# Performance work log

Measured on AMD Instinct MI355X. Metric: run time of the kernel, lower is better.

Reference implementation:

```python
import jax, jax.numpy as jnp
import numpy as np

N = 8192          # nodes
E = 262144        # edges (avg degree 32)
IN = 32           # output_seq_len * in_channels
HID = 16          # hidden_channels
HEADS = 8
OUT = 32          # output_seq_len * out_channels
SLOPE = 0.2       # GATv2 leaky_relu negative_slope
EPS = 1e-12       # F.normalize eps


def setup_inputs() -> dict:
    key = jax.random.key(0)
    ks = jax.random.split(key, 12)
    g = lambda k, shape, fan: (jax.random.normal(k, shape, jnp.float32) / np.float32(np.sqrt(fan)))
    x = jax.random.normal(ks[0], (N, IN), jnp.float32)
    edge_index = jax.random.randint(ks[1], (2, E), 0, N, dtype=jnp.int64)
    # conv1: in=IN -> HEADS x HID, concat
    W1l = g(ks[2], (IN, HEADS * HID), IN)
    b1l = jnp.zeros((HEADS * HID,), jnp.float32)
    W1r = g(ks[3], (IN, HEADS * HID), IN)
    b1r = jnp.zeros((HEADS * HID,), jnp.float32)
    att1 = g(ks[4], (HEADS, HID), HID)
    bias1 = jnp.zeros((HEADS * HID,), jnp.float32)
    W2l = g(ks[5], (HEADS * HID, OUT), HEADS * HID)
    b2l = jnp.zeros((OUT,), jnp.float32)
    W2r = g(ks[6], (HEADS * HID, OUT), HEADS * HID)
    b2r = jnp.zeros((OUT,), jnp.float32)
    att2 = g(ks[7], (1, OUT), OUT)
    bias2 = jnp.zeros((OUT,), jnp.float32)
    return {"x": x, "edge_index": edge_index,
            "W1l": W1l, "b1l": b1l, "W1r": W1r, "b1r": b1r, "att1": att1, "bias1": bias1,
            "W2l": W2l, "b2l": b2l, "W2r": W2r, "b2r": b2r, "att2": att2, "bias2": bias2}


def gatv2_conv(x, src, dst, Wl, bl, Wr, br, att, bias, heads, C, concat):
    """GATv2Conv (eval mode, self-loops already in src/dst). x: [N, F]."""
    n = x.shape[0]
    xl = (x @ Wl + bl).reshape(n, heads, C)  # source transform
    xr = (x @ Wr + br).reshape(n, heads, C)  # target transform
    h = jax.nn.leaky_relu(xl[src] + xr[dst], SLOPE)        # [Etot, H, C]
    e = jnp.einsum('ehc,hc->eh', h, att)                    # [Etot, H]
    m = jax.ops.segment_max(e, dst, num_segments=n)         # stable softmax per target
    p = jnp.exp(e - m[dst])
    s = jax.ops.segment_sum(p, dst, num_segments=n)
    alpha = p / (s[dst] + 1e-16)                            # [Etot, H]
    out = jax.ops.segment_sum(alpha[:, :, None] * xl[src], dst, num_segments=n)  # [n, H, C]
    out = out.reshape(n, heads * C) if concat else out.mean(axis=1)
    return out + bias


def reference(x, edge_index, W1l, b1l, W1r, b1r, att1, bias1, W2l, b2l, W2r, b2r, att2, bias2):
    n = x.shape[0]
    loops = jnp.arange(n, dtype=edge_index.dtype)
    src = jnp.concatenate([edge_index[0], loops])
    dst = jnp.concatenate([edge_index[1], loops])
    h1 = gatv2_conv(x, src, dst, W1l, b1l, W1r, b1r, att1, bias1, HEADS, HID, True)
    h2 = gatv2_conv(h1, src, dst, W2l, b2l, W2r, b2r, att2, bias2, 1, OUT, False)
    norm = jnp.sqrt(jnp.sum(h2 * h2, axis=1, keepdims=True))
    z = h2 / jnp.maximum(norm, EPS)                         # F.normalize(p=2, dim=1)
    A_pred = jax.nn.sigmoid(z @ z.T)                        # [N, N]
    return (A_pred, z)
```

## Files before the change

### kernel.cpp

```cpp
#include <hip/hip_runtime.h>
#include <hip/hip_bf16.h>
#include <cstdint>
#include <cstddef>

typedef float f32x4 __attribute__((ext_vector_type(4)));
typedef short short8 __attribute__((ext_vector_type(8)));

#define SLOT_SHIFT 7

__device__ __forceinline__ float bf2f(ushort u){ return __uint_as_float(((unsigned)u) << 16); }
__device__ __forceinline__ float lrelu(float v){ return fmaxf(v, 0.2f*v); }

__global__ __launch_bounds__(128) void k_linear1(const float* __restrict__ x,
                          const float* __restrict__ W1l, const float* __restrict__ b1l,
                          const float* __restrict__ W1r, const float* __restrict__ b1r,
                          __hip_bfloat16* __restrict__ xl1b, float* __restrict__ xr1,
                          int* __restrict__ cur, int N){
  __shared__ float xs[16][32];
  int t = threadIdx.x;
  int gid = blockIdx.x*128 + t;
  if (gid < N) cur[gid] = gid << SLOT_SHIFT;
  int r0 = blockIdx.x * 16;
  float wl[32], wr[32];
  #pragma unroll
  for (int k = 0; k < 32; k++){ wl[k] = W1l[k*128 + t]; wr[k] = W1r[k*128 + t]; }
  float bl = b1l[t], br = b1r[t];
  #pragma unroll
  for (int i = 0; i < 4; i++){
    int idx = t + i*128;
    xs[idx >> 5][idx & 31] = x[r0*32 + idx];
  }
  __syncthreads();
  #pragma unroll 4
  for (int r = 0; r < 16; r++){
    float al = bl, ar = br;
    const float4* xv4 = (const float4*)xs[r];
    #pragma unroll
    for (int q = 0; q < 8; q++){
      float4 xv = xv4[q];
      al += xv.x*wl[q*4+0] + xv.y*wl[q*4+1] + xv.z*wl[q*4+2] + xv.w*wl[q*4+3];
      ar += xv.x*wr[q*4+0] + xv.y*wr[q*4+1] + xv.z*wr[q*4+2] + xv.w*wr[q*4+3];
    }
    xl1b[(size_t)(r0+r)*128 + t] = __float2bfloat16(al);
    xr1[(size_t)(r0+r)*128 + t] = ar;
  }
}

__global__ void k_scatter(const int* __restrict__ ei, int E, int N,
                          int* __restrict__ cur, int* __restrict__ ssrc){
  int i = blockIdx.x*blockDim.x + threadIdx.x;
  int tot = E + N;
  if (i >= tot) return;
  int s = (i < E) ? ei[i]     : (i - E);
  int d = (i < E) ? ei[E + i] : (i - E);
  int pos = atomicAdd(&cur[d], 1);
  ssrc[pos] = s;
}

__global__ __launch_bounds__(256) void k_conv1l2(const int* __restrict__ cur,
                       const int* __restrict__ ssrc,
                       const __hip_bfloat16* __restrict__ xl1b, const float* __restrict__ xr1,
                       const float* __restrict__ att1, const float* __restrict__ bias1,
                       const float* __restrict__ W2l, const float* __restrict__ b2l,
                       const float* __restrict__ W2r, const float* __restrict__ b2r,
                       __hip_bfloat16* __restrict__ xl2b, float* __restrict__ xr2){
  __shared__ float p_s[2][128][8];
  __shared__ float h1s[8][128];
  int t = threadIdx.x;
  int sub = t >> 7, f = t & 127;
  int hp = f & 7;
  const ushort* xb = (const ushort*)xl1b;
  float4 attr0 = *(const float4*)(att1 + hp*16);
  float4 attr1 = *(const float4*)(att1 + hp*16 + 4);
  float4 attr2 = *(const float4*)(att1 + hp*16 + 8);
  float4 attr3 = *(const float4*)(att1 + hp*16 + 12);
  float b1f = bias1[f];
  int d0 = blockIdx.x*8;
  #pragma unroll
  for (int it = 0; it < 4; it++){
    int d = d0 + it*2 + sub;
    int j0 = d << SLOT_SHIFT;
    int deg = cur[d] - j0;
    float4 xr0 = *(const float4*)(xr1 + (size_t)d*128 + hp*16);
    float4 xr1v = *(const float4*)(xr1 + (size_t)d*128 + hp*16 + 4);
    float4 xr2v = *(const float4*)(xr1 + (size_t)d*128 + hp*16 + 8);
    float4 xr3v = *(const float4*)(xr1 + (size_t)d*128 + hp*16 + 12);
    __syncthreads();
    int npair = deg*8;
    for (int pr = f; pr < npair; pr += 128){
      int jj = pr >> 3;
      int src = ssrc[j0 + jj];
      const short8* vp = (const short8*)(xb + (size_t)src*128 + hp*16);
      short8 v0 = vp[0], v1 = vp[1];
      float e, tv = 0.f;
      e = bf2f((ushort)v0[0]) + xr0.x;  tv += lrelu(e)*attr0.x;
      e = bf2f((ushort)v0[1]) + xr0.y;  tv += lrelu(e)*attr0.y;
      e = bf2f((ushort)v0[2]) + xr0.z;  tv += lrelu(e)*attr0.z;
      e = bf2f((ushort)v0[3]) + xr0.w;  tv += lrelu(e)*attr0.w;
      e = bf2f((ushort)v0[4]) + xr1v.x; tv += lrelu(e)*attr1.x;
      e = bf2f((ushort)v0[5]) + xr1v.y; tv += lrelu(e)*attr1.y;
      e = bf2f((ushort)v0[6]) + xr1v.z; tv += lrelu(e)*attr1.z;
      e = bf2f((ushort)v0[7]) + xr1v.w; tv += lrelu(e)*attr1.w;
      e = bf2f((ushort)v1[0]) + xr2v.x; tv += lrelu(e)*attr2.x;
      e = bf2f((ushort)v1[1]) + xr2v.y; tv += lrelu(e)*attr2.y;
      e = bf2f((ushort)v1[2]) + xr2v.z; tv += lrelu(e)*attr2.z;
      e = bf2f((ushort)v1[3]) + xr2v.w; tv += lrelu(e)*attr2.w;
      e = bf2f((ushort)v1[4]) + xr3v.x; tv += lrelu(e)*attr3.x;
      e = bf2f((ushort)v1[5]) + xr3v.y; tv += lrelu(e)*attr3.y;
      e = bf2f((ushort)v1[6]) + xr3v.z; tv += lrelu(e)*attr3.z;
      e = bf2f((ushort)v1[7]) + xr3v.w; tv += lrelu(e)*attr3.w;
      p_s[sub][jj][hp] = __expf(tv);
    }
    __syncthreads();
    int h2 = f >> 4;
    float s = 0.f, acc = 0.f;
    int jj = 0;
    for (; jj + 3 < deg; jj += 4){
      int4 s4 = *(const int4*)&ssrc[j0 + jj];
      float p0 = p_s[sub][jj+0][h2];
      float p1 = p_s[sub][jj+1][h2];
      float p2 = p_s[sub][jj+2][h2];
      float p3 = p_s[sub][jj+3][h2];
      float x0 = bf2f(xb[(size_t)s4.x*128 + f]);
      float x1 = bf2f(xb[(size_t)s4.y*128 + f]);
      float x2 = bf2f(xb[(size_t)s4.z*128 + f]);
      float x3 = bf2f(xb[(size_t)s4.w*128 + f]);
      s   += (p0 + p1) + (p2 + p3);
      acc += p0*x0 + p1*x1 + p2*x2 + p3*x3;
    }
    for (; jj < deg; jj++){
      int src = ssrc[j0 + jj];
      float p = p_s[sub][jj][h2];
      float x = bf2f(xb[(size_t)src*128 + f]);
      s += p; acc += p*x;
    }
    h1s[it*2 + sub][f] = acc/(s + 1e-16f) + b1f;
  }
  __syncthreads();
  #pragma unroll
  for (int k = 0; k < 2; k++){
    int oo = t + k*256;
    int r = oo >> 6;
    int idx = oo & 63;
    int c = idx & 31; bool left = idx < 32;
    const float* W = left ? W2l : W2r;
    float a = left ? b2l[c] : b2r[c];
    #pragma unroll 8
    for (int kk = 0; kk < 128; kk++) a += h1s[r][kk] * W[kk*32 + c];
    int d = d0 + r;
    if (left) xl2b[(size_t)d*32 + c] = __float2bfloat16(a);
    else      xr2[(size_t)d*32 + c] = a;
  }
}

__global__ __launch_bounds__(256) void k_conv2(const int* __restrict__ cur,
                       const int* __restrict__ ssrc,
                       const __hip_bfloat16* __restrict__ xl2b, const float* __restrict__ xr2,
                       const float* __restrict__ att2, const float* __restrict__ bias2,
                       float* __restrict__ z, __hip_bfloat16* __restrict__ zb){
  __shared__ float p_s[4][128];
  __shared__ float xr_s[4][32];
  __shared__ float att_s[32];
  int t = threadIdx.x;
  int w = t >> 6, lane = t & 63;
  int d = blockIdx.x*4 + w;
  int j0 = d << SLOT_SHIFT;
  int deg = cur[d] - j0;
  if (t < 32) att_s[t] = att2[t];
  if (lane < 32) xr_s[w][lane] = xr2[(size_t)d*32 + lane];
  __syncthreads();
  const ushort* xb = (const ushort*)xl2b;
  for (int jj = lane; jj < deg; jj += 64){
    int src = ssrc[j0 + jj];
    const short8* vp = (const short8*)(xb + (size_t)src*32);
    short8 v0 = vp[0], v1 = vp[1], v2 = vp[2], v3 = vp[3];
    float tv = 0.f;
    #pragma unroll
    for (int k = 0; k < 8; k++){
      float e0 = bf2f((ushort)v0[k]) + xr_s[w][k];      tv += lrelu(e0)*att_s[k];
      float e1 = bf2f((ushort)v1[k]) + xr_s[w][8+k];    tv += lrelu(e1)*att_s[8+k];
      float e2 = bf2f((ushort)v2[k]) + xr_s[w][16+k];   tv += lrelu(e2)*att_s[16+k];
      float e3 = bf2f((ushort)v3[k]) + xr_s[w][24+k];   tv += lrelu(e3)*att_s[24+k];
    }
    p_s[w][jj] = __expf(tv);
  }
  __syncthreads();
  int half = lane >> 5, c = lane & 31;
  float s0 = 0.f, a0 = 0.f, s1 = 0.f, a1 = 0.f;
  int jj = half;
  for (; jj + 2 < deg; jj += 4){
    int srcA = ssrc[j0 + jj], srcB = ssrc[j0 + jj + 2];
    float pA = p_s[w][jj], pB = p_s[w][jj+2];
    float xA = bf2f(xb[(size_t)srcA*32 + c]);
    float xB = bf2f(xb[(size_t)srcB*32 + c]);
    s0 += pA; a0 += pA*xA;
    s1 += pB; a1 += pB*xB;
  }
  for (; jj < deg; jj += 2){
    int src = ssrc[j0 + jj];
    float p = p_s[w][jj];
    float x = bf2f(xb[(size_t)src*32 + c]);
    s0 += p; a0 += p*x;
  }
  float s = s0 + s1, acc = a0 + a1;
  s   += __shfl_xor(s, 32, 64);
  acc += __shfl_xor(acc, 32, 64);
  float v = acc/(s + 1e-16f) + bias2[c];
  float ss = v*v;
  #pragma unroll
  for (int k = 1; k < 32; k <<= 1) ss += __shfl_xor(ss, k, 64);
  if (half == 0){
    float zv = v / fmaxf(sqrtf(ss), 1e-12f);
    z[(size_t)d*32 + c] = zv;
    zb[(size_t)d*32 + c] = __float2bfloat16(zv);
  }
}

__global__ __launch_bounds__(256) void k_adj(const __hip_bfloat16* __restrict__ zb,
                                             float* __restrict__ out, int N){
  __shared__ float tile[64][68];
  int tid = threadIdx.x;
  int w = tid >> 6, l = tid & 63;
  int hi = l >> 4, lo = l & 15;
  int r0 = blockIdx.y*64, c0 = blockIdx.x*64;
  short8 a = *(const short8*)(zb + (size_t)(r0 + w*16 + lo)*32 + hi*8);
  f32x4 acc[4];
  #pragma unroll
  for (int ct = 0; ct < 4; ct++){
    short8 b = *(const short8*)(zb + (size_t)(c0 + ct*16 + lo)*32 + hi*8);
    acc[ct] = __builtin_amdgcn_mfma_f32_16x16x32_bf16(a, b, (f32x4){0.f,0.f,0.f,0.f}, 0, 0, 0);
  }
  #pragma unroll
  for (int ct = 0; ct < 4; ct++){
    #pragma unroll
    for (int r = 0; r < 4; r++)
      tile[w*16 + hi*4 + r][ct*16 + lo] = 1.f/(1.f + __expf(-acc[ct][r]));
  }
  __syncthreads();
  #pragma unroll
  for (int k = 0; k < 4; k++){
    int g = tid + k*256;
    int row = g >> 4, c4 = (g & 15)*4;
    f32x4 v = *(const f32x4*)&tile[row][c4];
    *(f32x4*)&out[(size_t)(r0 + row)*N + c0 + c4] = v;
  }
}

extern "C" void kernel_launch(void* const* d_in, const int* in_sizes, int n_in,
                              void* d_out, int out_size, void* d_ws, size_t ws_size,
                              hipStream_t stream){
  const float* x     = (const float*)d_in[0];
  const int*   ei    = (const int*)  d_in[1];
  const float* W1l   = (const float*)d_in[2];
  const float* b1l   = (const float*)d_in[3];
  const float* W1r   = (const float*)d_in[4];
  const float* b1r   = (const float*)d_in[5];
  const float* att1  = (const float*)d_in[6];
  const float* bias1 = (const float*)d_in[7];
  const float* W2l   = (const float*)d_in[8];
  const float* b2l   = (const float*)d_in[9];
  const float* W2r   = (const float*)d_in[10];
  const float* b2r   = (const float*)d_in[11];
  const float* att2  = (const float*)d_in[12];
  const float* bias2 = (const float*)d_in[13];

  const int N = in_sizes[0] / 32;
  const int E = in_sizes[1] / 2;
  const int Etot = E + N;

  char* w = (char*)d_ws;
  size_t p = 0;
  auto take = [&](size_t bytes)->char*{
    char* r = w + p;
    p = (p + bytes + 255) & ~(size_t)255;
    return r;
  };
  int*   cur  = (int*)  take((size_t)N*4);
  int*   ssrc = (int*)  take(((size_t)N << SLOT_SHIFT)*4);
  __hip_bfloat16* xl1b = (__hip_bfloat16*)take((size_t)N*128*2);
  float* xr1  = (float*)take((size_t)N*128*4);
  __hip_bfloat16* xl2b = (__hip_bfloat16*)take((size_t)N*32*2);
  float* xr2  = (float*)take((size_t)N*32*4);
  __hip_bfloat16* zb = (__hip_bfloat16*)take((size_t)N*32*2);

  float* Apred = (float*)d_out;
  float* z     = Apred + (size_t)N*N;

  k_linear1<<<N/16, 128, 0, stream>>>(x, W1l, b1l, W1r, b1r, xl1b, xr1, cur, N);
  k_scatter<<<(Etot+255)/256, 256, 0, stream>>>(ei, E, N, cur, ssrc);
  k_conv1l2<<<N/8, 256, 0, stream>>>(cur, ssrc, xl1b, xr1, att1, bias1,
                                     W2l, b2l, W2r, b2r, xl2b, xr2);
  k_conv2  <<<N/4, 256, 0, stream>>>(cur, ssrc, xl2b, xr2, att2, bias2, z, zb);

  dim3 grid(N/64, N/64);
  k_adj    <<<grid, 256, 0, stream>>>(zb, Apred, N);
}
```

Measured before the change: 125.1 us.

## Fuse linear1 with edge scatter, stage neighbor indices in LDS, halve conv1 nodes per block

Merges the first linear transform and the CSR-style edge scatter into one launch whose blocks are partitioned by index, with the per-node counters zeroed by a memset instead of being initialized inside the linear kernel. Both conv kernels now copy each node's neighbor index list into shared memory once, so the score pass and the aggregation pass read it from LDS rather than global memory. The conv1 kernel handles 4 nodes per block instead of 8, doubling the grid to improve occupancy and load balance. The cost is an extra memset launch and additional LDS usage and barriers per node.

```diff
diff --git a/kernel.cpp b/kernel.cpp
--- a/kernel.cpp
+++ b/kernel.cpp
@@ -11,53 +11,54 @@
 __device__ __forceinline__ float bf2f(ushort u){ return __uint_as_float(((unsigned)u) << 16); }
 __device__ __forceinline__ float lrelu(float v){ return fmaxf(v, 0.2f*v); }
 
-__global__ __launch_bounds__(128) void k_linear1(const float* __restrict__ x,
+__global__ __launch_bounds__(256) void k_lin1_scatter(const float* __restrict__ x,
                           const float* __restrict__ W1l, const float* __restrict__ b1l,
                           const float* __restrict__ W1r, const float* __restrict__ b1r,
                           __hip_bfloat16* __restrict__ xl1b, float* __restrict__ xr1,
-                          int* __restrict__ cur, int N){
-  __shared__ float xs[16][32];
-  int t = threadIdx.x;
-  int gid = blockIdx.x*128 + t;
-  if (gid < N) cur[gid] = gid << SLOT_SHIFT;
-  int r0 = blockIdx.x * 16;
-  float wl[32], wr[32];
-  #pragma unroll
-  for (int k = 0; k < 32; k++){ wl[k] = W1l[k*128 + t]; wr[k] = W1r[k*128 + t]; }
-  float bl = b1l[t], br = b1r[t];
-  #pragma unroll
-  for (int i = 0; i < 4; i++){
-    int idx = t + i*128;
-    xs[idx >> 5][idx & 31] = x[r0*32 + idx];
-  }
-  __syncthreads();
-  #pragma unroll 4
-  for (int r = 0; r < 16; r++){
-    float al = bl, ar = br;
-    const float4* xv4 = (const float4*)xs[r];
+                          const int* __restrict__ ei, int E, int N,
+                          int* __restrict__ cnt, int* __restrict__ ssrc, int NL){
+  int bid = blockIdx.x, t = threadIdx.x;
+  if (bid < NL){
+    __shared__ float xs[32][32];
+    int sub = t >> 7, f = t & 127;
+    int r0 = bid*32;
+    float wl[32], wr[32];
     #pragma unroll
-    for (int q = 0; q < 8; q++){
-      float4 xv = xv4[q];
-      al += xv.x*wl[q*4+0] + xv.y*wl[q*4+1] + xv.z*wl[q*4+2] + xv.w*wl[q*4+3];
-      ar += xv.x*wr[q*4+0] + xv.y*wr[q*4+1] + xv.z*wr[q*4+2] + xv.w*wr[q*4+3];
-    }
-    xl1b[(size_t)(r0+r)*128 + t] = __float2bfloat16(al);
-    xr1[(size_t)(r0+r)*128 + t] = ar;
-  }
-}
-
-__global__ void k_scatter(const int* __restrict__ ei, int E, int N,
-                          int* __restrict__ cur, int* __restrict__ ssrc){
-  int i = blockIdx.x*blockDim.x + threadIdx.x;
-  int tot = E + N;
-  if (i >= tot) return;
-  int s = (i < E) ? ei[i]     : (i - E);
-  int d = (i < E) ? ei[E + i] : (i - E);
-  int pos = atomicAdd(&cur[d], 1);
-  ssrc[pos] = s;
-}
-
-__global__ __launch_bounds__(256) void k_conv1l2(const int* __restrict__ cur,
+    for (int k = 0; k < 32; k++){ wl[k] = W1l[k*128 + f]; wr[k] = W1r[k*128 + f]; }
+    float bl = b1l[f], br = b1r[f];
+    #pragma unroll
+    for (int i = 0; i < 4; i++){
+      int idx = t + i*256;
+      xs[idx >> 5][idx & 31] = x[r0*32 + idx];
+    }
+    __syncthreads();
+    #pragma unroll 4
+    for (int rr = 0; rr < 16; rr++){
+      int r = sub*16 + rr;
+      float al = bl, ar = br;
+      const float4* xv4 = (const float4*)xs[r];
+      #pragma unroll
+      for (int q = 0; q < 8; q++){
+        float4 xv = xv4[q];
+        al += xv.x*wl[q*4+0] + xv.y*wl[q*4+1] + xv.z*wl[q*4+2] + xv.w*wl[q*4+3];
+        ar += xv.x*wr[q*4+0] + xv.y*wr[q*4+1] + xv.z*wr[q*4+2] + xv.w*wr[q*4+3];
+      }
+      xl1b[(size_t)(r0+r)*128 + f] = __float2bfloat16(al);
+      xr1[(size_t)(r0+r)*128 + f] = ar;
+    }
+  } else {
+    int i = (bid - NL)*256 + t;
+    int tot = E + N;
+    if (i < tot){
+      int s = (i < E) ? ei[i]     : (i - E);
+      int d = (i < E) ? ei[E + i] : (i - E);
+      int pos = atomicAdd(&cnt[d], 1);
+      ssrc[(d << SLOT_SHIFT) + pos] = s;
+    }
+  }
+}
+
+__global__ __launch_bounds__(256) void k_conv1l2(const int* __restrict__ cnt,
                        const int* __restrict__ ssrc,
                        const __hip_bfloat16* __restrict__ xl1b, const float* __restrict__ xr1,
                        const float* __restrict__ att1, const float* __restrict__ bias1,
@@ -65,7 +66,8 @@
                        const float* __restrict__ W2r, const float* __restrict__ b2r,
                        __hip_bfloat16* __restrict__ xl2b, float* __restrict__ xr2){
   __shared__ float p_s[2][128][8];
-  __shared__ float h1s[8][128];
+  __shared__ int   sj[2][128];
+  __shared__ float h1s[4][128];
   int t = threadIdx.x;
   int sub = t >> 7, f = t & 127;
   int hp = f & 7;
@@ -75,28 +77,30 @@
   float4 attr2 = *(const float4*)(att1 + hp*16 + 8);
   float4 attr3 = *(const float4*)(att1 + hp*16 + 12);
   float b1f = bias1[f];
-  int d0 = blockIdx.x*8;
-  #pragma unroll
-  for (int it = 0; it < 4; it++){
+  int d0 = blockIdx.x*4;
+  #pragma unroll
+  for (int it = 0; it < 2; it++){
     int d = d0 + it*2 + sub;
     int j0 = d << SLOT_SHIFT;
-    int deg = cur[d] - j0;
-    float4 xr0 = *(const float4*)(xr1 + (size_t)d*128 + hp*16);
+    int deg = cnt[d];
+    float4 xr0v = *(const float4*)(xr1 + (size_t)d*128 + hp*16);
     float4 xr1v = *(const float4*)(xr1 + (size_t)d*128 + hp*16 + 4);
     float4 xr2v = *(const float4*)(xr1 + (size_t)d*128 + hp*16 + 8);
     float4 xr3v = *(const float4*)(xr1 + (size_t)d*128 + hp*16 + 12);
     __syncthreads();
+    for (int i = f; i < deg; i += 128) sj[sub][i] = ssrc[j0 + i];
+    __syncthreads();
     int npair = deg*8;
     for (int pr = f; pr < npair; pr += 128){
       int jj = pr >> 3;
-      int src = ssrc[j0 + jj];
+      int src = sj[sub][jj];
       const short8* vp = (const short8*)(xb + (size_t)src*128 + hp*16);
       short8 v0 = vp[0], v1 = vp[1];
       float e, tv = 0.f;
-      e = bf2f((ushort)v0[0]) + xr0.x;  tv += lrelu(e)*attr0.x;
-      e = bf2f((ushort)v0[1]) + xr0.y;  tv += lrelu(e)*attr0.y;
-      e = bf2f((ushort)v0[2]) + xr0.z;  tv += lrelu(e)*attr0.z;
-      e = bf2f((ushort)v0[3]) + xr0.w;  tv += lrelu(e)*attr0.w;
+      e = bf2f((ushort)v0[0]) + xr0v.x; tv += lrelu(e)*attr0.x;
+      e = bf2f((ushort)v0[1]) + xr0v.y; tv += lrelu(e)*attr0.y;
+      e = bf2f((ushort)v0[2]) + xr0v.z; tv += lrelu(e)*attr0.z;
+      e = bf2f((ushort)v0[3]) + xr0v.w; tv += lrelu(e)*attr0.w;
       e = bf2f((ushort)v0[4]) + xr1v.x; tv += lrelu(e)*attr1.x;
       e = bf2f((ushort)v0[5]) + xr1v.y; tv += lrelu(e)*attr1.y;
       e = bf2f((ushort)v0[6]) + xr1v.z; tv += lrelu(e)*attr1.z;
@@ -116,7 +120,7 @@
     float s = 0.f, acc = 0.f;
     int jj = 0;
     for (; jj + 3 < deg; jj += 4){
-      int4 s4 = *(const int4*)&ssrc[j0 + jj];
+      int4 s4 = *(const int4*)&sj[sub][jj];
       float p0 = p_s[sub][jj+0][h2];
       float p1 = p_s[sub][jj+1][h2];
       float p2 = p_s[sub][jj+2][h2];
@@ -129,7 +133,7 @@
       acc += p0*x0 + p1*x1 + p2*x2 + p3*x3;
     }
     for (; jj < deg; jj++){
-      int src = ssrc[j0 + jj];
+      int src = sj[sub][jj];
       float p = p_s[sub][jj][h2];
       float x = bf2f(xb[(size_t)src*128 + f]);
       s += p; acc += p*x;
@@ -137,11 +141,9 @@
     h1s[it*2 + sub][f] = acc/(s + 1e-16f) + b1f;
   }
   __syncthreads();
-  #pragma unroll
-  for (int k = 0; k < 2; k++){
-    int oo = t + k*256;
-    int r = oo >> 6;
-    int idx = oo & 63;
+  {
+    int r = t >> 6;
+    int idx = t & 63;
     int c = idx & 31; bool left = idx < 32;
     const float* W = left ? W2l : W2r;
     float a = left ? b2l[c] : b2r[c];
@@ -153,25 +155,27 @@
   }
 }
 
-__global__ __launch_bounds__(256) void k_conv2(const int* __restrict__ cur,
+__global__ __launch_bounds__(256) void k_conv2(const int* __restrict__ cnt,
                        const int* __restrict__ ssrc,
                        const __hip_bfloat16* __restrict__ xl2b, const float* __restrict__ xr2,
                        const float* __restrict__ att2, const float* __restrict__ bias2,
                        float* __restrict__ z, __hip_bfloat16* __restrict__ zb){
   __shared__ float p_s[4][128];
+  __shared__ int   sj[4][128];
   __shared__ float xr_s[4][32];
   __shared__ float att_s[32];
   int t = threadIdx.x;
   int w = t >> 6, lane = t & 63;
   int d = blockIdx.x*4 + w;
   int j0 = d << SLOT_SHIFT;
-  int deg = cur[d] - j0;
+  int deg = cnt[d];
   if (t < 32) att_s[t] = att2[t];
   if (lane < 32) xr_s[w][lane] = xr2[(size_t)d*32 + lane];
   __syncthreads();
   const ushort* xb = (const ushort*)xl2b;
   for (int jj = lane; jj < deg; jj += 64){
     int src = ssrc[j0 + jj];
+    sj[w][jj] = src;
     const short8* vp = (const short8*)(xb + (size_t)src*32);
     short8 v0 = vp[0], v1 = vp[1], v2 = vp[2], v3 = vp[3];
     float tv = 0.f;
@@ -189,7 +193,7 @@
   float s0 = 0.f, a0 = 0.f, s1 = 0.f, a1 = 0.f;
   int jj = half;
   for (; jj + 2 < deg; jj += 4){
-    int srcA = ssrc[j0 + jj], srcB = ssrc[j0 + jj + 2];
+    int srcA = sj[w][jj], srcB = sj[w][jj+2];
     float pA = p_s[w][jj], pB = p_s[w][jj+2];
     float xA = bf2f(xb[(size_t)srcA*32 + c]);
     float xB = bf2f(xb[(size_t)srcB*32 + c]);
@@ -197,7 +201,7 @@
     s1 += pB; a1 += pB*xB;
   }
   for (; jj < deg; jj += 2){
-    int src = ssrc[j0 + jj];
+    int src = sj[w][jj];
     float p = p_s[w][jj];
     float x = bf2f(xb[(size_t)src*32 + c]);
     s0 += p; a0 += p*x;
@@ -275,7 +279,7 @@
     p = (p + bytes + 255) & ~(size_t)255;
     return r;
   };
-  int*   cur  = (int*)  take((size_t)N*4);
+  int*   cnt  = (int*)  take((size_t)N*4);
   int*   ssrc = (int*)  take(((size_t)N << SLOT_SHIFT)*4);
   __hip_bfloat16* xl1b = (__hip_bfloat16*)take((size_t)N*128*2);
   float* xr1  = (float*)take((size_t)N*128*4);
@@ -286,11 +290,14 @@
   float* Apred = (float*)d_out;
   float* z     = Apred + (size_t)N*N;
 
-  k_linear1<<<N/16, 128, 0, stream>>>(x, W1l, b1l, W1r, b1r, xl1b, xr1, cur, N);
-  k_scatter<<<(Etot+255)/256, 256, 0, stream>>>(ei, E, N, cur, ssrc);
-  k_conv1l2<<<N/8, 256, 0, stream>>>(cur, ssrc, xl1b, xr1, att1, bias1,
+  const int NL = N/32;
+  const int NS = (Etot + 255)/256;
+  (void)hipMemsetAsync(cnt, 0, (size_t)N*4, stream);
+  k_lin1_scatter<<<NL + NS, 256, 0, stream>>>(x, W1l, b1l, W1r, b1r, xl1b, xr1,
+                                              ei, E, N, cnt, ssrc, NL);
+  k_conv1l2<<<N/4, 256, 0, stream>>>(cnt, ssrc, xl1b, xr1, att1, bias1,
                                      W2l, b2l, W2r, b2r, xl2b, xr2);
-  k_conv2  <<<N/4, 256, 0, stream>>>(cur, ssrc, xl2b, xr2, att2, bias2, z, zb);
+  k_conv2  <<<N/4, 256, 0, stream>>>(cnt, ssrc, xl2b, xr2, att2, bias2, z, zb);
 
   dim3 grid(N/64, N/64);
   k_adj    <<<grid, 256, 0, stream>>>(zb, Apred, N);
```

New measurement: 113.7 us. -9.1%, faster.
